# Performance work log

Hardware: AMD Instinct MI355X
Metric: run time of the kernel (lower is better)

The kernel has to match this reference:

```python
import jax, jax.numpy as jnp
import numpy as np

N_NODES = 100000
N_EDGES = 3200000
FEATURE = 128
HIDDEN = 128
N_LAYERS = 3


def _glorot(key, fan_in, fan_out):
    lim = np.sqrt(6.0 / (fan_in + fan_out)).astype(np.float32)
    return jax.random.uniform(key, (fan_in, fan_out), jnp.float32, -lim, lim)


def setup_inputs() -> dict:
    key = jax.random.key(0)
    ks = jax.random.split(key, 8)
    x = jax.random.normal(ks[0], (N_NODES, FEATURE), jnp.float32)
    edge_index = jax.random.randint(ks[1], (2, N_EDGES), 0, N_NODES, jnp.int64)
    W0 = _glorot(ks[2], FEATURE, HIDDEN)
    W1 = _glorot(ks[3], HIDDEN, HIDDEN)
    W2 = _glorot(ks[4], HIDDEN, HIDDEN)
    b0 = jnp.zeros((HIDDEN,), jnp.float32)
    b1 = jnp.zeros((HIDDEN,), jnp.float32)
    b2 = jnp.zeros((HIDDEN,), jnp.float32)
    return {"x": x, "edge_index": edge_index,
            "W0": W0, "b0": b0, "W1": W1, "b1": b1, "W2": W2, "b2": b2}


def _gcn_conv(x, W, b, src, dst, n):
    # PyG GCNConv: linear -> add self loops -> sym-norm aggregate -> +bias
    h = x @ W  # [N, H]
    loop = jnp.arange(n)
    s = jnp.concatenate([src, loop])  # sources incl. self loops
    d = jnp.concatenate([dst, loop])  # targets incl. self loops
    deg = jax.ops.segment_sum(jnp.ones_like(d, dtype=h.dtype), d, num_segments=n)
    dinv = jnp.where(deg > 0, jax.lax.rsqrt(jnp.maximum(deg, 1.0)), 0.0)
    norm = dinv[s] * dinv[d]  # [E+N]
    out = jax.ops.segment_sum(h[s] * norm[:, None], d, num_segments=n)
    return out + b


def reference(x, edge_index, W0, b0, W1, b1, W2, b2):
    # forward of GCN: (GCNConv -> relu -> dropout[eval=no-op]) x layer
    src, dst = edge_index[0], edge_index[1]
    n = x.shape[0]
    for W, b in ((W0, b0), (W1, b1), (W2, b2)):
        x = jax.nn.relu(_gcn_conv(x, W, b, src, dst, n))
    return x
```

## Files before the change

kernel.cpp:

```cpp
#include <hip/hip_runtime.h>
#include <hip/hip_fp16.h>

#define N_NODES 100000
#define N_EDGES 3200000
#define NBUCKETS 391
#define NCHUNKB 256
#define CHUNK 12500

typedef __attribute__((ext_vector_type(8))) short sh8;
typedef __attribute__((ext_vector_type(4))) float fl4;

__device__ inline void split_bf16(float x, short& hi, short& lo) {
    unsigned u = __float_as_uint(x);
    unsigned r = u + 0x7FFFu + ((u >> 16) & 1u);
    hi = (short)(r >> 16);
    float hif = __uint_as_float(r & 0xFFFF0000u);
    float lof = x - hif;
    unsigned u2 = __float_as_uint(lof);
    lo = (short)((u2 + 0x7FFFu + ((u2 >> 16) & 1u)) >> 16);
}


__global__ __launch_bounds__(256) void k_bhist(const int* __restrict__ ei_dst,
                                               int* __restrict__ bucket_cnt) {
    __shared__ int h[NBUCKETS];
    int t = threadIdx.x;
    for (int i = t; i < NBUCKETS; i += 256) h[i] = 0;
    __syncthreads();
    int base = blockIdx.x * CHUNK;
    for (int i = t; i < CHUNK; i += 256)
        atomicAdd(&h[ei_dst[base + i] >> 8], 1);
    __syncthreads();
    for (int i = t; i < NBUCKETS; i += 256)
        if (h[i]) atomicAdd(&bucket_cnt[i], h[i]);
}

__global__ __launch_bounds__(512) void k_bscan(const int* __restrict__ bucket_cnt,
                                               int* __restrict__ bucket_base,
                                               int* __restrict__ bucket_fill) {
    __shared__ int s[512];
    int t = threadIdx.x;
    int v = (t < NBUCKETS) ? bucket_cnt[t] : 0;
    s[t] = v;
    __syncthreads();
    for (int off = 1; off < 512; off <<= 1) {
        int x = (t >= off) ? s[t - off] : 0;
        __syncthreads();
        s[t] += x;
        __syncthreads();
    }
    int ex = s[t] - v;
    if (t < NBUCKETS) { bucket_base[t] = ex; bucket_fill[t] = ex; }
    if (t == NBUCKETS - 1) bucket_base[NBUCKETS] = s[t];
}

__global__ __launch_bounds__(256) void k_bscatter(const int* __restrict__ ei,
                                                  int* __restrict__ bucket_fill,
                                                  unsigned* __restrict__ bpairs) {
    __shared__ int h[NBUCKETS];
    __shared__ int basep[NBUCKETS];
    int t = threadIdx.x;
    const int* dstp = ei + N_EDGES;
    int base = blockIdx.x * CHUNK;

    for (int i = t; i < NBUCKETS; i += 256) h[i] = 0;
    __syncthreads();
    for (int i = t; i < CHUNK; i += 256)
        atomicAdd(&h[dstp[base + i] >> 8], 1);
    __syncthreads();
    for (int i = t; i < NBUCKETS; i += 256) {
        int c = h[i];
        basep[i] = c ? atomicAdd(&bucket_fill[i], c) : 0;
    }
    __syncthreads();
    for (int i = t; i < NBUCKETS; i += 256) h[i] = 0;
    __syncthreads();
    for (int i = t; i < CHUNK; i += 256) {
        int d = dstp[base + i];
        int s = ei[base + i];
        int b = d >> 8;
        int r = atomicAdd(&h[b], 1);
        bpairs[basep[b] + r] = (unsigned)s | ((unsigned)(d & 255) << 17);
    }
}

__global__ __launch_bounds__(256) void k_bbuild(const unsigned* __restrict__ bpairs,
                                                const int* __restrict__ bucket_base,
                                                int* __restrict__ row_ptr,
                                                int* __restrict__ cnt,
                                                float* __restrict__ dinv,
                                                int* __restrict__ csr_src) {
    __shared__ int h[256];
    __shared__ int sc[256];
    int b = blockIdx.x;
    int t = threadIdx.x;
    int e0 = bucket_base[b], e1 = bucket_base[b + 1];

    h[t] = 0;
    __syncthreads();
    for (int i = e0 + t; i < e1; i += 256)
        atomicAdd(&h[bpairs[i] >> 17], 1);
    __syncthreads();
    int v = h[t];
    sc[t] = v;
    __syncthreads();
    for (int off = 1; off < 256; off <<= 1) {
        int x = (t >= off) ? sc[t - off] : 0;
        __syncthreads();
        sc[t] += x;
        __syncthreads();
    }
    int ex = sc[t] - v;
    int node = b * 256 + t;
    if (node < N_NODES) {
        cnt[node] = v;
        dinv[node] = rsqrtf((float)(v + 1));
        row_ptr[node] = e0 + ex;
    }
    __syncthreads();
    h[t] = e0 + ex;
    __syncthreads();
    for (int i = e0 + t; i < e1; i += 256) {
        unsigned p = bpairs[i];
        int pos = atomicAdd(&h[p >> 17], 1);
        csr_src[pos] = (int)(p & 0x1FFFFu);
    }
}


__global__ __launch_bounds__(256) void k_wprep(const float* __restrict__ W0,
                                               const float* __restrict__ W1,
                                               const float* __restrict__ W2,
                                               short* __restrict__ fhi,
                                               short* __restrict__ flo,
                                               int* __restrict__ bucket_cnt) {
    if (blockIdx.x == 192) {
        for (int i = threadIdx.x; i < NBUCKETS; i += 256) bucket_cnt[i] = 0;
        return;
    }
    int idx = blockIdx.x * 256 + threadIdx.x;
    int l = idx >> 14, e = idx & 16383;
    const float* W = (l == 0) ? W0 : (l == 1) ? W1 : W2;
    float w = W[e];
    int k = e >> 7, n = e & 127;
    int ks = k >> 5, q = (k >> 3) & 3, j = k & 7;
    int c = n >> 4, n16 = n & 15;
    int lane = q * 16 + n16;
    int dst = ((l * 32 + ks * 8 + c) * 64 + lane) * 8 + j;
    short hi, lo;
    split_bf16(w, hi, lo);
    fhi[dst] = hi;
    flo[dst] = lo;
}


__global__ __launch_bounds__(512, 4) void k_gemm_mfma(const float* __restrict__ X,
                                                      const short* __restrict__ fhi,
                                                      const short* __restrict__ flo,
                                                      const float* __restrict__ dinv,
                                                      __half* __restrict__ H16) {
    __shared__ short Bh[16384];
    __shared__ short Bl[16384];

    int t = threadIdx.x;
    int wave = t >> 6, lane = t & 63;
    int q = lane >> 4, n16 = lane & 15;
    int row_base = blockIdx.x * 128 + wave * 16;

    int r0 = row_base + n16;
    if (r0 > N_NODES - 1) r0 = N_NODES - 1;
    const float* p0 = X + (long long)r0 * 128 + q * 8;
    float4 a[4][2];
#pragma unroll
    for (int ks = 0; ks < 4; ++ks) {
        a[ks][0] = *(const float4*)(p0 + ks * 32);
        a[ks][1] = *(const float4*)(p0 + ks * 32 + 4);
    }

    {
        const float4* sh_ = (const float4*)fhi;
        const float4* sl_ = (const float4*)flo;
        float4* dh = (float4*)Bh;
        float4* dl = (float4*)Bl;
#pragma unroll
        for (int i = 0; i < 4; ++i) {
            dh[t + i * 512] = sh_[t + i * 512];
            dl[t + i * 512] = sl_[t + i * 512];
        }
    }

    sh8 ah[4], al[4];
#pragma unroll
    for (int ks = 0; ks < 4; ++ks) {
        float xs[8];
        xs[0] = a[ks][0].x; xs[1] = a[ks][0].y; xs[2] = a[ks][0].z; xs[3] = a[ks][0].w;
        xs[4] = a[ks][1].x; xs[5] = a[ks][1].y; xs[6] = a[ks][1].z; xs[7] = a[ks][1].w;
#pragma unroll
        for (int j = 0; j < 8; ++j) {
            short h, l;
            split_bf16(xs[j], h, l);
            ah[ks][j] = h;
            al[ks][j] = l;
        }
    }

    fl4 acc[8];
#pragma unroll
    for (int c = 0; c < 8; ++c) acc[c] = (fl4){0.f, 0.f, 0.f, 0.f};

    __syncthreads();

#pragma unroll
    for (int ks = 0; ks < 4; ++ks)
#pragma unroll
        for (int c = 0; c < 8; ++c) {
            sh8 bh = *(const sh8*)&Bh[((ks * 8 + c) * 64 + lane) * 8];
            sh8 bl = *(const sh8*)&Bl[((ks * 8 + c) * 64 + lane) * 8];
            acc[c] = __builtin_amdgcn_mfma_f32_16x16x32_bf16(ah[ks], bh, acc[c], 0, 0, 0);
            acc[c] = __builtin_amdgcn_mfma_f32_16x16x32_bf16(al[ks], bh, acc[c], 0, 0, 0);
            acc[c] = __builtin_amdgcn_mfma_f32_16x16x32_bf16(ah[ks], bl, acc[c], 0, 0, 0);
        }

#pragma unroll
    for (int reg = 0; reg < 4; ++reg) {
        int grow = row_base + q * 4 + reg;
        if (grow < N_NODES) {
            float sc = dinv[grow];
            __half* dst = H16 + (long long)grow * 128 + n16;
#pragma unroll
            for (int c = 0; c < 8; ++c)
                dst[c * 16] = __float2half(acc[c][reg] * sc);
        }
    }
}


__global__ __launch_bounds__(256) void k_gather(const __half2* __restrict__ H2,
                                                const int* __restrict__ csr_src,
                                                const int* __restrict__ row_ptr,
                                                const int* __restrict__ cnt,
                                                const float* __restrict__ dinv,
                                                const float* __restrict__ b,
                                                float* __restrict__ out) {
    int wv = __builtin_amdgcn_readfirstlane(threadIdx.x >> 6);
    int node = blockIdx.x * 4 + wv;
    int lane = threadIdx.x & 63;
    if (node >= N_NODES) return;

    int start = row_ptr[node];
    int n = cnt[node];

    float2 self_ = __half22float2(H2[node * 64 + lane]);
    float accx = self_.x, accy = self_.y;

    int j = 0;
    for (; j + 8 <= n; j += 8) {
        int s[8];
#pragma unroll
        for (int u = 0; u < 8; ++u) s[u] = csr_src[start + j + u];
        float2 h[8];
#pragma unroll
        for (int u = 0; u < 8; ++u) h[u] = __half22float2(H2[s[u] * 64 + lane]);
#pragma unroll
        for (int u = 0; u < 8; ++u) { accx += h[u].x; accy += h[u].y; }
    }
    for (; j < n; ++j) {
        float2 h = __half22float2(H2[csr_src[start + j] * 64 + lane]);
        accx += h.x; accy += h.y;
    }

    float dd = dinv[node];
    float2 bb = ((const float2*)b)[lane];
    float2 v;
    v.x = fmaxf(fmaf(accx, dd, bb.x), 0.0f);
    v.y = fmaxf(fmaf(accy, dd, bb.y), 0.0f);
    ((float2*)out)[node * 64 + lane] = v;
}


extern "C" void kernel_launch(void* const* d_in, const int* in_sizes, int n_in,
                              void* d_out, int out_size, void* d_ws, size_t ws_size,
                              hipStream_t stream) {
    const float* x  = (const float*)d_in[0];
    const int*   ei = (const int*)d_in[1];
    const float* Wm[3] = {(const float*)d_in[2], (const float*)d_in[4], (const float*)d_in[6]};
    const float* bv[3] = {(const float*)d_in[3], (const float*)d_in[5], (const float*)d_in[7]};
    float* out = (float*)d_out;

    char* w = (char*)d_ws;
    int*      row_ptr     = (int*)(w + 0);
    int*      cnt         = (int*)(w + 400384);
    float*    dinv        = (float*)(w + 800768);
    int*      bucket_cnt  = (int*)(w + 1201152);
    int*      bucket_base = (int*)(w + 1203200);
    int*      bucket_fill = (int*)(w + 1205248);
    unsigned* bpairs      = (unsigned*)(w + 1207296);
    int*      csr_src     = (int*)(w + 14007808);
    short*    fragHi      = (short*)(w + 26808320);
    short*    fragLo      = (short*)(w + 26906624);
    __half*   H16         = (__half*)(w + 27004928);

    k_wprep<<<193, 256, 0, stream>>>(Wm[0], Wm[1], Wm[2], fragHi, fragLo, bucket_cnt);
    k_bhist<<<NCHUNKB, 256, 0, stream>>>(ei + N_EDGES, bucket_cnt);
    k_bscan<<<1, 512, 0, stream>>>(bucket_cnt, bucket_base, bucket_fill);
    k_bscatter<<<NCHUNKB, 256, 0, stream>>>(ei, bucket_fill, bpairs);
    k_bbuild<<<NBUCKETS, 256, 0, stream>>>(bpairs, bucket_base, row_ptr, cnt, dinv, csr_src);

    const float* xin = x;
    for (int l = 0; l < 3; ++l) {
        k_gemm_mfma<<<(N_NODES + 127) / 128, 512, 0, stream>>>(xin, fragHi + l * 16384,
                                                               fragLo + l * 16384, dinv, H16);
        k_gather<<<(N_NODES + 3) / 4, 256, 0, stream>>>((const __half2*)H16, csr_src,
                                                        row_ptr, cnt, dinv, bv[l], out);
        xin = out;
    }
}
```

Measured before the change: 589.5 us.

## Slice features into 16-wide column planes for cache-local gather

The fp16 H buffer and the intermediate layer outputs now use a sliced layout of 8 planes, each holding 16 features for every node. The gather kernel gives each block one slice, and 8 groups of lanes split a node's edges between them, followed by a shuffle reduction. The aim is to shrink the per-slice working set (100k×32B = 3.2MB) so the random neighbour reads hit L2, at the cost of reading the edge indices 8 times and doing more index loads and shuffles. The GEMM reads the sliced input for layers 1 and 2, and only the last layer writes the standard row-major output.

```diff
diff --git a/kernel.cpp b/kernel.cpp
--- a/kernel.cpp
+++ b/kernel.cpp
@@ -9,6 +9,7 @@
 
 typedef __attribute__((ext_vector_type(8))) short sh8;
 typedef __attribute__((ext_vector_type(4))) float fl4;
+typedef __attribute__((ext_vector_type(2))) float f2v;
 
 __device__ inline void split_bf16(float x, short& hi, short& lo) {
     unsigned u = __float_as_uint(x);
@@ -158,7 +159,8 @@
                                                       const short* __restrict__ fhi,
                                                       const short* __restrict__ flo,
                                                       const float* __restrict__ dinv,
-                                                      __half* __restrict__ H16) {
+                                                      __half* __restrict__ H16,
+                                                      int sliced) {
     __shared__ short Bh[16384];
     __shared__ short Bl[16384];
 
@@ -169,12 +171,22 @@
 
     int r0 = row_base + n16;
     if (r0 > N_NODES - 1) r0 = N_NODES - 1;
-    const float* p0 = X + (long long)r0 * 128 + q * 8;
     float4 a[4][2];
-#pragma unroll
-    for (int ks = 0; ks < 4; ++ks) {
-        a[ks][0] = *(const float4*)(p0 + ks * 32);
-        a[ks][1] = *(const float4*)(p0 + ks * 32 + 4);
+    if (!sliced) {
+        const float* p0 = X + (long long)r0 * 128 + q * 8;
+#pragma unroll
+        for (int ks = 0; ks < 4; ++ks) {
+            a[ks][0] = *(const float4*)(p0 + ks * 32);
+            a[ks][1] = *(const float4*)(p0 + ks * 32 + 4);
+        }
+    } else {
+#pragma unroll
+        for (int ks = 0; ks < 4; ++ks) {
+            int sl = ks * 2 + (q >> 1);
+            const float* p = X + ((long long)sl * N_NODES + r0) * 16 + (q & 1) * 8;
+            a[ks][0] = *(const float4*)p;
+            a[ks][1] = *(const float4*)(p + 4);
+        }
     }
 
     {
@@ -226,10 +238,9 @@
         int grow = row_base + q * 4 + reg;
         if (grow < N_NODES) {
             float sc = dinv[grow];
-            __half* dst = H16 + (long long)grow * 128 + n16;
 #pragma unroll
             for (int c = 0; c < 8; ++c)
-                dst[c * 16] = __float2half(acc[c][reg] * sc);
+                H16[(c * N_NODES + grow) * 16 + n16] = __float2half(acc[c][reg] * sc);
         }
     }
 }
@@ -241,40 +252,57 @@
                                                 const int* __restrict__ cnt,
                                                 const float* __restrict__ dinv,
                                                 const float* __restrict__ b,
-                                                float* __restrict__ out) {
+                                                float* __restrict__ out,
+                                                int std_out) {
+    int s = blockIdx.x & 7;
+    int grp = blockIdx.x >> 3;
     int wv = __builtin_amdgcn_readfirstlane(threadIdx.x >> 6);
-    int node = blockIdx.x * 4 + wv;
     int lane = threadIdx.x & 63;
-    if (node >= N_NODES) return;
-
-    int start = row_ptr[node];
-    int n = cnt[node];
-
-    float2 self_ = __half22float2(H2[node * 64 + lane]);
-    float accx = self_.x, accy = self_.y;
-
-    int j = 0;
-    for (; j + 8 <= n; j += 8) {
-        int s[8];
-#pragma unroll
-        for (int u = 0; u < 8; ++u) s[u] = csr_src[start + j + u];
-        float2 h[8];
-#pragma unroll
-        for (int u = 0; u < 8; ++u) h[u] = __half22float2(H2[s[u] * 64 + lane]);
-#pragma unroll
-        for (int u = 0; u < 8; ++u) { accx += h[u].x; accy += h[u].y; }
-    }
-    for (; j < n; ++j) {
-        float2 h = __half22float2(H2[csr_src[start + j] * 64 + lane]);
-        accx += h.x; accy += h.y;
-    }
-
-    float dd = dinv[node];
-    float2 bb = ((const float2*)b)[lane];
-    float2 v;
-    v.x = fmaxf(fmaf(accx, dd, bb.x), 0.0f);
-    v.y = fmaxf(fmaf(accy, dd, bb.y), 0.0f);
-    ((float2*)out)[node * 64 + lane] = v;
+    int g8 = lane >> 3, f4 = lane & 7;
+    int sbase = s * N_NODES;
+    float2 bb = ((const float2*)b)[s * 8 + f4];
+
+    for (int k = 0; k < 4; ++k) {
+        int node = grp * 16 + wv * 4 + k;
+        int start = row_ptr[node];
+        int n = cnt[node];
+
+        float2 self_ = __half22float2(H2[(sbase + node) * 8 + f4]);
+        float accx = (g8 == 0) ? self_.x : 0.0f;
+        float accy = (g8 == 0) ? self_.y : 0.0f;
+
+        for (int j = 0; j < n; j += 32) {
+            int idx[4];
+#pragma unroll
+            for (int u = 0; u < 4; ++u) {
+                int e = j + u * 8 + g8;
+                idx[u] = (e < n) ? __builtin_nontemporal_load(csr_src + start + e) : -1;
+            }
+#pragma unroll
+            for (int u = 0; u < 4; ++u)
+                if (idx[u] >= 0) {
+                    float2 h = __half22float2(H2[(sbase + idx[u]) * 8 + f4]);
+                    accx += h.x; accy += h.y;
+                }
+        }
+
+#pragma unroll
+        for (int m = 8; m <= 32; m <<= 1) {
+            accx += __shfl_xor(accx, m, 64);
+            accy += __shfl_xor(accy, m, 64);
+        }
+
+        if (g8 == 0) {
+            float dd = dinv[node];
+            f2v v;
+            v.x = fmaxf(fmaf(accx, dd, bb.x), 0.0f);
+            v.y = fmaxf(fmaf(accy, dd, bb.y), 0.0f);
+            if (std_out)
+                __builtin_nontemporal_store(v, (f2v*)(out + node * 128 + s * 16) + f4);
+            else
+                __builtin_nontemporal_store(v, (f2v*)(out + (sbase + node) * 16) + f4);
+        }
+    }
 }
 
 
@@ -309,9 +337,11 @@
     const float* xin = x;
     for (int l = 0; l < 3; ++l) {
         k_gemm_mfma<<<(N_NODES + 127) / 128, 512, 0, stream>>>(xin, fragHi + l * 16384,
-                                                               fragLo + l * 16384, dinv, H16);
-        k_gather<<<(N_NODES + 3) / 4, 256, 0, stream>>>((const __half2*)H16, csr_src,
-                                                        row_ptr, cnt, dinv, bv[l], out);
+                                                               fragLo + l * 16384, dinv, H16,
+                                                               l > 0);
+        k_gather<<<8 * (N_NODES / 16), 256, 0, stream>>>((const __half2*)H16, csr_src,
+                                                         row_ptr, cnt, dinv, bv[l], out,
+                                                         l == 2);
         xin = out;
     }
 }
```

Result: slower. 1.310 ms (+122.2%).

## Gather neighbor rows with 16-byte loads across four edge sub-groups

Applied to the files above, without the earlier changes.

The gather kernel now splits each wavefront into four 16-lane groups. Each group loads a full 256-byte fp16 row with uint4 loads and handles a different neighbor, with four neighbors in flight per group. The next round's source indices are prefetched, out-of-range edges are masked with a zero multiplier, and partial sums are reduced across groups with shuffles. The goal is wider memory transactions and more memory-level parallelism in the bandwidth-bound SpMM. The cost is extra shuffles and wasted loads on the masked tail of each row.

```diff
diff --git a/kernel.cpp b/kernel.cpp
--- a/kernel.cpp
+++ b/kernel.cpp
@@ -235,7 +235,18 @@
 }
 
 
-__global__ __launch_bounds__(256) void k_gather(const __half2* __restrict__ H2,
+__device__ inline void acc8(const uint4& h, float m, float* a) {
+    float2 f0 = __half22float2(*(const __half2*)&h.x);
+    float2 f1 = __half22float2(*(const __half2*)&h.y);
+    float2 f2 = __half22float2(*(const __half2*)&h.z);
+    float2 f3 = __half22float2(*(const __half2*)&h.w);
+    a[0] = fmaf(f0.x, m, a[0]); a[1] = fmaf(f0.y, m, a[1]);
+    a[2] = fmaf(f1.x, m, a[2]); a[3] = fmaf(f1.y, m, a[3]);
+    a[4] = fmaf(f2.x, m, a[4]); a[5] = fmaf(f2.y, m, a[5]);
+    a[6] = fmaf(f3.x, m, a[6]); a[7] = fmaf(f3.y, m, a[7]);
+}
+
+__global__ __launch_bounds__(256) void k_gather(const __half* __restrict__ H,
                                                 const int* __restrict__ csr_src,
                                                 const int* __restrict__ row_ptr,
                                                 const int* __restrict__ cnt,
@@ -245,36 +256,74 @@
     int wv = __builtin_amdgcn_readfirstlane(threadIdx.x >> 6);
     int node = blockIdx.x * 4 + wv;
     int lane = threadIdx.x & 63;
+    int sub = lane >> 4;
+    int fc  = lane & 15;
     if (node >= N_NODES) return;
 
     int start = row_ptr[node];
     int n = cnt[node];
-
-    float2 self_ = __half22float2(H2[node * 64 + lane]);
-    float accx = self_.x, accy = self_.y;
-
-    int j = 0;
-    for (; j + 8 <= n; j += 8) {
-        int s[8];
-#pragma unroll
-        for (int u = 0; u < 8; ++u) s[u] = csr_src[start + j + u];
-        float2 h[8];
-#pragma unroll
-        for (int u = 0; u < 8; ++u) h[u] = __half22float2(H2[s[u] * 64 + lane]);
-#pragma unroll
-        for (int u = 0; u < 8; ++u) { accx += h[u].x; accy += h[u].y; }
-    }
-    for (; j < n; ++j) {
-        float2 h = __half22float2(H2[csr_src[start + j] * 64 + lane]);
-        accx += h.x; accy += h.y;
-    }
-
     float dd = dinv[node];
-    float2 bb = ((const float2*)b)[lane];
+    float2 bb = ((const float2*)b)[fc * 4 + sub];
+
+    const char* Hb = (const char*)H;
+
+    float acc[8];
+#pragma unroll
+    for (int i = 0; i < 8; ++i) acc[i] = 0.0f;
+
+    {
+        uint4 sr = *(const uint4*)(Hb + (size_t)node * 256 + fc * 16);
+        acc8(sr, (sub == 0) ? 1.0f : 0.0f, acc);
+    }
+
+    if (n > 0) {
+        int nm1 = n - 1;
+        int e;
+        int i0, i1, i2, i3;
+        e = sub;      i0 = csr_src[start + ((e < nm1) ? e : nm1)];
+        e = 4 + sub;  i1 = csr_src[start + ((e < nm1) ? e : nm1)];
+        e = 8 + sub;  i2 = csr_src[start + ((e < nm1) ? e : nm1)];
+        e = 12 + sub; i3 = csr_src[start + ((e < nm1) ? e : nm1)];
+
+        for (int j = 0; j < n; j += 16) {
+            uint4 h0 = *(const uint4*)(Hb + (size_t)(unsigned)i0 * 256 + fc * 16);
+            uint4 h1 = *(const uint4*)(Hb + (size_t)(unsigned)i1 * 256 + fc * 16);
+            uint4 h2 = *(const uint4*)(Hb + (size_t)(unsigned)i2 * 256 + fc * 16);
+            uint4 h3 = *(const uint4*)(Hb + (size_t)(unsigned)i3 * 256 + fc * 16);
+            int jn = j + 16;
+            int n0, n1, n2, n3;
+            e = jn + sub;      n0 = csr_src[start + ((e < nm1) ? e : nm1)];
+            e = jn + 4 + sub;  n1 = csr_src[start + ((e < nm1) ? e : nm1)];
+            e = jn + 8 + sub;  n2 = csr_src[start + ((e < nm1) ? e : nm1)];
+            e = jn + 12 + sub; n3 = csr_src[start + ((e < nm1) ? e : nm1)];
+            __builtin_amdgcn_sched_barrier(0);
+            float m0 = (j + sub      < n) ? 1.0f : 0.0f;
+            float m1 = (j + 4 + sub  < n) ? 1.0f : 0.0f;
+            float m2 = (j + 8 + sub  < n) ? 1.0f : 0.0f;
+            float m3 = (j + 12 + sub < n) ? 1.0f : 0.0f;
+            acc8(h0, m0, acc);
+            acc8(h1, m1, acc);
+            acc8(h2, m2, acc);
+            acc8(h3, m3, acc);
+            i0 = n0; i1 = n1; i2 = n2; i3 = n3;
+        }
+    }
+
+#pragma unroll
+    for (int i = 0; i < 8; ++i) {
+        acc[i] += __shfl_xor(acc[i], 16, 64);
+        acc[i] += __shfl_xor(acc[i], 32, 64);
+    }
+
+    float sx = acc[0], sy = acc[1];
+    if (sub == 1) { sx = acc[2]; sy = acc[3]; }
+    if (sub == 2) { sx = acc[4]; sy = acc[5]; }
+    if (sub == 3) { sx = acc[6]; sy = acc[7]; }
+
     float2 v;
-    v.x = fmaxf(fmaf(accx, dd, bb.x), 0.0f);
-    v.y = fmaxf(fmaf(accy, dd, bb.y), 0.0f);
-    ((float2*)out)[node * 64 + lane] = v;
+    v.x = fmaxf(fmaf(sx, dd, bb.x), 0.0f);
+    v.y = fmaxf(fmaf(sy, dd, bb.y), 0.0f);
+    ((float2*)out)[node * 64 + fc * 4 + sub] = v;
 }
 
 
@@ -310,7 +359,7 @@
     for (int l = 0; l < 3; ++l) {
         k_gemm_mfma<<<(N_NODES + 127) / 128, 512, 0, stream>>>(xin, fragHi + l * 16384,
                                                                fragLo + l * 16384, dinv, H16);
-        k_gather<<<(N_NODES + 3) / 4, 256, 0, stream>>>((const __half2*)H16, csr_src,
+        k_gather<<<(N_NODES + 3) / 4, 256, 0, stream>>>(H16, csr_src,
                                                         row_ptr, cnt, dinv, bv[l], out);
         xin = out;
     }
```

After: 588.6 us, median of 2. Within noise of the previous version (-0.1%).
